# Performance work log

Measured on AMD Instinct MI355X. Metric: run time of the kernel, lower is better.

Reference implementation:

```python
import jax, jax.numpy as jnp
import numpy as np

C = 192
NUM_HEADS = 4
K = 3
KV_STRIDE = 2
EPS = 1e-5


def _conv(x, w, stride, groups):
    # x: [B,C,H,W], w: [O, I//groups, kh, kw]
    return jax.lax.conv_general_dilated(
        x, w, window_strides=(stride, stride),
        padding=[(K // 2, K // 2), (K // 2, K // 2)] if w.shape[-1] > 1 else [(0, 0), (0, 0)],
        dimension_numbers=("NCHW", "OIHW", "NCHW"),
        feature_group_count=groups)


def _bn(x, gamma, beta, mean, var):
    # eval-mode batchnorm over channel dim of NCHW
    inv = gamma / jnp.sqrt(var + EPS)
    return x * inv[None, :, None, None] + (beta - mean * inv)[None, :, None, None]


def _dwconv_flatten(x, dw, g, b, m, v, pw, stride):
    y = _conv(x, dw, stride, groups=C)          # depthwise
    y = _bn(y, g, b, m, v)
    y = _conv(y, pw, 1, groups=1)               # 1x1 pointwise
    B, O, h, w = y.shape
    return y.reshape(B, O, h * w).transpose(0, 2, 1)  # b (h w) c


def setup_inputs() -> dict:
    key = jax.random.key(0)
    ks = jax.random.split(key, 16)
    B, H, W = 8, 56, 56
    d = {
        "x": jax.random.normal(ks[0], (B, H * W, C), jnp.float32),
        "H": H,
        "W": W,
        "dw_q": jax.random.normal(ks[1], (C, 1, K, K), jnp.float32) * 0.1,
        "bn_q_gamma": jax.random.uniform(ks[2], (C,), jnp.float32, 0.5, 1.5),
        "bn_q_beta": jax.random.normal(ks[3], (C,), jnp.float32) * 0.1,
        "bn_q_mean": jax.random.normal(ks[4], (C,), jnp.float32) * 0.1,
        "bn_q_var": jax.random.uniform(ks[5], (C,), jnp.float32, 0.5, 1.5),
        "pw_q": jax.random.normal(ks[6], (C, C, 1, 1), jnp.float32) * (1.0 / np.sqrt(C)),
        "dw_kv": jax.random.normal(ks[7], (C, 1, K, K), jnp.float32) * 0.1,
        "bn_kv_gamma": jax.random.uniform(ks[8], (C,), jnp.float32, 0.5, 1.5),
        "bn_kv_beta": jax.random.normal(ks[9], (C,), jnp.float32) * 0.1,
        "bn_kv_mean": jax.random.normal(ks[10], (C,), jnp.float32) * 0.1,
        "bn_kv_var": jax.random.uniform(ks[11], (C,), jnp.float32, 0.5, 1.5),
        "pw_kv": jax.random.normal(ks[12], (2 * C, C, 1, 1), jnp.float32) * (1.0 / np.sqrt(C)),
        "Wq": jax.random.normal(ks[13], (C, C), jnp.float32) * (1.0 / np.sqrt(C)),
        "bq": jnp.zeros((C,), jnp.float32),
        "Wk": jax.random.normal(ks[14], (C, C), jnp.float32) * (1.0 / np.sqrt(C)),
        "bk": jnp.zeros((C,), jnp.float32),
        "Wv": jax.random.normal(ks[15], (C, C), jnp.float32) * (1.0 / np.sqrt(C)),
        "bv": jnp.zeros((C,), jnp.float32),
    }
    return d


def reference(x, H, W, dw_q, bn_q_gamma, bn_q_beta, bn_q_mean, bn_q_var, pw_q,
              dw_kv, bn_kv_gamma, bn_kv_beta, bn_kv_mean, bn_kv_var, pw_kv,
              Wq, bq, Wk, bk, Wv, bv):
    B, N, _ = x.shape
    h = NUM_HEADS
    hd = C // h
    scale = hd ** -0.5
    # Token2Patch: b (H W) c -> b c H W
    xp = x.transpose(0, 2, 1).reshape(B, C, H, W)
    conv_q = _dwconv_flatten(xp, dw_q, bn_q_gamma, bn_q_beta, bn_q_mean, bn_q_var, pw_q, 1)  # [B,N,C]
    kv = _dwconv_flatten(xp, dw_kv, bn_kv_gamma, bn_kv_beta, bn_kv_mean, bn_kv_var, pw_kv, KV_STRIDE)  # [B,M,2C]
    conv_k, conv_v = kv[..., :C], kv[..., C:]
    q = (conv_q @ Wq.T + bq).reshape(B, N, h, hd).transpose(0, 2, 1, 3)      # [B,h,N,hd]
    M = conv_k.shape[1]
    k = (conv_k @ Wk.T + bk).reshape(B, M, h, hd).transpose(0, 2, 1, 3)      # [B,h,M,hd]
    v = (conv_v @ Wv.T + bv).reshape(B, M, h, hd).transpose(0, 2, 1, 3)      # [B,h,M,hd]
    attn = jnp.einsum("bhnd,bhmd->bhnm", q, k) * scale
    attn = jax.nn.softmax(attn, axis=-1)
    out = jnp.einsum("bhnm,bhmd->bhnd", attn, v)
    # MergeHeads: b h n d -> b n (h d)
    return out.transpose(0, 2, 1, 3).reshape(B, N, C)
```

## Files before the change

### kernel.cpp

```cpp
#include <hip/hip_runtime.h>
#include <cmath>

typedef _Float16 f16;
typedef _Float16 f16x8 __attribute__((ext_vector_type(8)));
typedef _Float16 f16x4 __attribute__((ext_vector_type(4)));
typedef float    f32x4 __attribute__((ext_vector_type(4)));
typedef unsigned int u32;
typedef u32 u32x2 __attribute__((ext_vector_type(2)));

#define C_   192
#define HH   56
#define WW   56
#define NN   3136
#define BB   8
#define MM   784
#define NHEAD 4
#define HD   48
#define VT_LD 832
#define KVPB (BB*MM/32)

#define MFMA16(a,b,c)  __builtin_amdgcn_mfma_f32_16x16x32_f16(a,b,c,0,0,0)
#define MFMAK16(a,b,c) __builtin_amdgcn_mfma_f32_16x16x16f16(a,b,c,0,0,0)

static __device__ __forceinline__ u32 pkrtz(float a, float b) {
    typedef __fp16 fp16x2 __attribute__((ext_vector_type(2)));
    fp16x2 h = __builtin_amdgcn_cvt_pkrtz(a, b);
    return __builtin_bit_cast(u32, h);
}

static __device__ __forceinline__ void gload16(const void* g, void* l) {
    __builtin_amdgcn_global_load_lds(
        (const __attribute__((address_space(1))) unsigned int*)g,
        (__attribute__((address_space(3))) unsigned int*)l, 16, 0, 0);
}

__device__ __forceinline__ void dwbn_oct(
    const float* __restrict__ x, const float* __restrict__ dwL,
    const float* __restrict__ gamma, const float* __restrict__ beta,
    const float* __restrict__ mean,  const float* __restrict__ var,
    f16* __restrict__ out, int idx)
{
    int c4 = idx % 48;
    int r1 = idx / 48;
    int qx = r1 % (WW/4);
    int r2 = r1 / (WW/4);
    int qp = r2 % (HH/2);
    int b  = r2 / (HH/2);
    int c0 = c4*4;

    float4 w4[9];
    #pragma unroll
    for (int j = 0; j < 9; ++j)
        w4[j] = *(const float4*)&dwL[c4*40 + j*4];
    const float* wf = (const float*)w4;

    float4 g4  = *(const float4*)(gamma + c0);
    float4 be4 = *(const float4*)(beta + c0);
    float4 m4  = *(const float4*)(mean + c0);
    float4 v4  = *(const float4*)(var  + c0);

    float4 acc[2][4];
    #pragma unroll
    for (int jj = 0; jj < 2; ++jj)
        #pragma unroll
        for (int ii = 0; ii < 4; ++ii)
            acc[jj][ii] = make_float4(0.f,0.f,0.f,0.f);

    int iyTop = 2*qp - 1;
    int ix0   = 4*qx - 1;
    #pragma unroll
    for (int j = 0; j < 4; ++j) {
        int iy = iyTop + j;
        if (iy < 0 || iy >= HH) continue;
        #pragma unroll
        for (int i = 0; i < 6; ++i) {
            int ix = ix0 + i;
            if (ix < 0 || ix >= WW) continue;
            float4 xv = *reinterpret_cast<const float4*>(
                x + ((size_t)b*NN + iy*WW + ix)*C_ + c0);
            #pragma unroll
            for (int jj = 0; jj < 2; ++jj) {
                if (j < jj || j > jj+2) continue;
                #pragma unroll
                for (int ii = 0; ii < 4; ++ii) {
                    if (i < ii || i > ii+2) continue;
                    const int wi = (j-jj)*3 + (i-ii);
                    acc[jj][ii].x = fmaf(wf[ 0+wi], xv.x, acc[jj][ii].x);
                    acc[jj][ii].y = fmaf(wf[ 9+wi], xv.y, acc[jj][ii].y);
                    acc[jj][ii].z = fmaf(wf[18+wi], xv.z, acc[jj][ii].z);
                    acc[jj][ii].w = fmaf(wf[27+wi], xv.w, acc[jj][ii].w);
                }
            }
        }
    }
    float i0 = g4.x*__frsqrt_rn(v4.x + 1e-5f);
    float i1 = g4.y*__frsqrt_rn(v4.y + 1e-5f);
    float i2 = g4.z*__frsqrt_rn(v4.z + 1e-5f);
    float i3 = g4.w*__frsqrt_rn(v4.w + 1e-5f);
    float b0 = be4.x - m4.x*i0, b1 = be4.y - m4.y*i1;
    float b2 = be4.z - m4.z*i2, b3 = be4.w - m4.w*i3;
    #pragma unroll
    for (int jj = 0; jj < 2; ++jj) {
        #pragma unroll
        for (int ii = 0; ii < 4; ++ii) {
            f16x4 r;
            r[0] = (f16)(acc[jj][ii].x*i0 + b0);
            r[1] = (f16)(acc[jj][ii].y*i1 + b1);
            r[2] = (f16)(acc[jj][ii].z*i2 + b2);
            r[3] = (f16)(acc[jj][ii].w*i3 + b3);
            size_t o = (((size_t)b*HH + 2*qp + jj)*WW + 4*qx + ii)*48 + c4;
            *reinterpret_cast<f16x4*>(out + o*4) = r;
        }
    }
}

__device__ __forceinline__ void dwbn_quad2(
    const float* __restrict__ x, const float* __restrict__ dwL,
    const float* __restrict__ gamma, const float* __restrict__ beta,
    const float* __restrict__ mean,  const float* __restrict__ var,
    f16* __restrict__ out, int idx)
{
    const int OH = 28, OW = 28, STRIDE = 2;
    int c4 = idx % 48;
    int r1 = idx / 48;
    int qx = r1 % (OW/2);
    int r2 = r1 / (OW/2);
    int qp = r2 % (OH/2);
    int b  = r2 / (OH/2);
    int c0 = c4*4;

    float4 w4[9];
    #pragma unroll
    for (int j = 0; j < 9; ++j)
        w4[j] = *(const float4*)&dwL[c4*40 + j*4];
    const float* wf = (const float*)w4;

    float4 g4  = *(const float4*)(gamma + c0);
    float4 be4 = *(const float4*)(beta + c0);
    float4 m4  = *(const float4*)(mean + c0);
    float4 v4  = *(const float4*)(var  + c0);

    float4 a00 = make_float4(0.f,0.f,0.f,0.f);
    float4 a01 = a00, a10 = a00, a11 = a00;
    int iyTop = (2*qp)*STRIDE - 1;
    int ix0   = (2*qx)*STRIDE - 1;
    #pragma unroll
    for (int j = 0; j < STRIDE+3; ++j) {
        int iy = iyTop + j;
        if (iy < 0 || iy >= HH) continue;
        #pragma unroll
        for (int i = 0; i < STRIDE+3; ++i) {
            int ix = ix0 + i;
            if (ix < 0 || ix >= WW) continue;
            float4 xv = *reinterpret_cast<const float4*>(
                x + ((size_t)b*NN + iy*WW + ix)*C_ + c0);
            const bool r0ok = (j <= 2), r1ok = (j >= STRIDE);
            const bool c0ok = (i <= 2), c1ok = (i >= STRIDE);
            if (r0ok && c0ok) { const int wi = j*3 + i;
                a00.x = fmaf(wf[ 0+wi], xv.x, a00.x);
                a00.y = fmaf(wf[ 9+wi], xv.y, a00.y);
                a00.z = fmaf(wf[18+wi], xv.z, a00.z);
                a00.w = fmaf(wf[27+wi], xv.w, a00.w); }
            if (r0ok && c1ok) { const int wi = j*3 + (i-STRIDE);
                a01.x = fmaf(wf[ 0+wi], xv.x, a01.x);
                a01.y = fmaf(wf[ 9+wi], xv.y, a01.y);
                a01.z = fmaf(wf[18+wi], xv.z, a01.z);
                a01.w = fmaf(wf[27+wi], xv.w, a01.w); }
            if (r1ok && c0ok) { const int wi = (j-STRIDE)*3 + i;
                a10.x = fmaf(wf[ 0+wi], xv.x, a10.x);
                a10.y = fmaf(wf[ 9+wi], xv.y, a10.y);
                a10.z = fmaf(wf[18+wi], xv.z, a10.z);
                a10.w = fmaf(wf[27+wi], xv.w, a10.w); }
            if (r1ok && c1ok) { const int wi = (j-STRIDE)*3 + (i-STRIDE);
                a11.x = fmaf(wf[ 0+wi], xv.x, a11.x);
                a11.y = fmaf(wf[ 9+wi], xv.y, a11.y);
                a11.z = fmaf(wf[18+wi], xv.z, a11.z);
                a11.w = fmaf(wf[27+wi], xv.w, a11.w); }
        }
    }
    float i0 = g4.x*__frsqrt_rn(v4.x + 1e-5f);
    float i1 = g4.y*__frsqrt_rn(v4.y + 1e-5f);
    float i2 = g4.z*__frsqrt_rn(v4.z + 1e-5f);
    float i3 = g4.w*__frsqrt_rn(v4.w + 1e-5f);
    float b0 = be4.x - m4.x*i0, b1 = be4.y - m4.y*i1;
    float b2 = be4.z - m4.z*i2, b3 = be4.w - m4.w*i3;
    size_t base = (((size_t)b*OH + 2*qp)*OW + 2*qx)*48 + c4;
    f16x4 r;
    r[0]=(f16)(a00.x*i0+b0); r[1]=(f16)(a00.y*i1+b1);
    r[2]=(f16)(a00.z*i2+b2); r[3]=(f16)(a00.w*i3+b3);
    *reinterpret_cast<f16x4*>(out + base*4) = r;
    r[0]=(f16)(a01.x*i0+b0); r[1]=(f16)(a01.y*i1+b1);
    r[2]=(f16)(a01.z*i2+b2); r[3]=(f16)(a01.w*i3+b3);
    *reinterpret_cast<f16x4*>(out + (base + 48)*4) = r;
    r[0]=(f16)(a10.x*i0+b0); r[1]=(f16)(a10.y*i1+b1);
    r[2]=(f16)(a10.z*i2+b2); r[3]=(f16)(a10.w*i3+b3);
    *reinterpret_cast<f16x4*>(out + (base + (size_t)OW*48)*4) = r;
    r[0]=(f16)(a11.x*i0+b0); r[1]=(f16)(a11.y*i1+b1);
    r[2]=(f16)(a11.z*i2+b2); r[3]=(f16)(a11.w*i3+b3);
    *reinterpret_cast<f16x4*>(out + (base + (size_t)OW*48 + 48)*4) = r;
}

__global__ __launch_bounds__(256) void prep_all(
    const float* __restrict__ x,
    const float* __restrict__ dwq,  const float* __restrict__ gq,
    const float* __restrict__ bq_,  const float* __restrict__ mq,
    const float* __restrict__ vq,
    const float* __restrict__ dwkv, const float* __restrict__ gkv,
    const float* __restrict__ bkv,  const float* __restrict__ mkv,
    const float* __restrict__ vkv,
    const float* __restrict__ Wq, const float* __restrict__ Wk,
    const float* __restrict__ Wv, const float* __restrict__ pw_q,
    const float* __restrict__ pw_kv,
    f16* __restrict__ uq, f16* __restrict__ ukv,
    f16* __restrict__ Mq, f16* __restrict__ Mk, f16* __restrict__ Mv,
    f16* __restrict__ vt)
{
    int blk = blockIdx.x, tid = threadIdx.x;
    const int QB = 588, KB = 294;
    if (blk < QB + KB) {
        bool qp = blk < QB;
        __shared__ __align__(16) float dwL[48*40];
        const float* dwg = qp ? dwq : dwkv;
        for (int i = tid; i < 432; i += 256) {
            int f  = i*4;
            int c4 = f/36, r = f%36;
            *(float4*)&dwL[c4*40 + r] = *(const float4*)(dwg + f);
        }
        __syncthreads();
        if (qp)
            dwbn_oct(x, dwL, gq, bq_, mq, vq, uq, blk*256 + tid);
        else
            dwbn_quad2(x, dwL, gkv, bkv, mkv, vkv, ukv, (blk - QB)*256 + tid);
    } else if (blk < QB + KB + 576) {
        int fb = blk - QB - KB;
        int which = fb / 192, o = fb % 192;
        const float* Wm = which == 0 ? Wq : (which == 1 ? Wk : Wv);
        const float* P  = which == 0 ? pw_q : (which == 1 ? pw_kv : pw_kv + C_*C_);
        f16* Mo         = which == 0 ? Mq : (which == 1 ? Mk : Mv);
        __shared__ float wrow[C_];
        if (tid < C_) wrow[tid] = Wm[o*C_ + tid];
        __syncthreads();
        if (tid < C_) {
            float acc = 0.f;
            #pragma unroll 8
            for (int j = 0; j < C_; ++j)
                acc = fmaf(wrow[j], P[j*C_ + tid], acc);
            Mo[o*C_ + tid] = (f16)acc;
        }
    } else {
        int i = (blk - QB - KB - 576)*256 + tid;
        int b = i / (C_*48);
        int rem = i % (C_*48);
        int c = rem / 48;
        int m = MM + (rem % 48);
        vt[((size_t)b*C_ + c)*VT_LD + m] = (f16)0.f;
    }
}

__global__ __launch_bounds__(128, 1) void proj_kv(
    const f16* __restrict__ ukv,
    const f16* __restrict__ Mk, const f16* __restrict__ Mv,
    const float* __restrict__ bk, const float* __restrict__ bv,
    f16* __restrict__ kb, f16* __restrict__ vt)
{
    int tid  = threadIdx.x;
    int w    = tid >> 6, l = tid & 63;
    int lrow = l & 15,  lgrp = l >> 4;
    int blk  = blockIdx.x;
    int path = blk < KVPB ? 1 : 2;
    int rblk = path == 1 ? blk : blk - KVPB;
    int r0 = rblk*32 + w*16;

    const f16* urow = ukv + (size_t)(r0 + lrow)*C_;
    f16x8 a[6];
    #pragma unroll
    for (int ch = 0; ch < 6; ++ch)
        a[ch] = *(const f16x8*)(urow + ch*32 + lgrp*8);

    f16x8 bfA[6], bfB[6];
    const f16* Mm = path == 1 ? Mk : Mv;

    #pragma unroll
    for (int ch = 0; ch < 6; ++ch)
        bfA[ch] = *(const f16x8*)(Mm + (size_t)lrow*C_ + ch*32 + lgrp*8);

    if (path == 1) {
        #pragma unroll
        for (int ct = 0; ct < 12; ++ct) {
            f16x8* cur = (ct & 1) ? bfB : bfA;
            f16x8* nxt = (ct & 1) ? bfA : bfB;
            if (ct < 11) {
                const f16* mrow = Mm + (size_t)((ct+1)*16 + lrow)*C_;
                #pragma unroll
                for (int ch = 0; ch < 6; ++ch)
                    nxt[ch] = *(const f16x8*)(mrow + ch*32 + lgrp*8);
            }
            f32x4 acc = {0.f,0.f,0.f,0.f};
            #pragma unroll
            for (int ch = 0; ch < 6; ++ch)
                acc = MFMA16(cur[ch], a[ch], acc);
            float4 bo = *(const float4*)(bk + ct*16 + lgrp*4);
            f16x4 st;
            st[0] = (f16)(acc[0] + bo.x);
            st[1] = (f16)(acc[1] + bo.y);
            st[2] = (f16)(acc[2] + bo.z);
            st[3] = (f16)(acc[3] + bo.w);
            *(f16x4*)(kb + (size_t)(r0 + lrow)*C_ + ct*16 + lgrp*4) = st;
        }
    } else {
        #pragma unroll
        for (int ct = 0; ct < 12; ++ct) {
            f16x8* cur = (ct & 1) ? bfB : bfA;
            f16x8* nxt = (ct & 1) ? bfA : bfB;
            if (ct < 11) {
                const f16* mrow = Mv + (size_t)((ct+1)*16 + lrow)*C_;
                #pragma unroll
                for (int ch = 0; ch < 6; ++ch)
                    nxt[ch] = *(const f16x8*)(mrow + ch*32 + lgrp*8);
            }
            int o = ct*16 + lrow;
            f32x4 acc = {0.f,0.f,0.f,0.f};
            #pragma unroll
            for (int ch = 0; ch < 6; ++ch)
                acc = MFMA16(a[ch], cur[ch], acc);
            float bo = bv[o];
            int rg = r0 + lgrp*4;
            int b  = rg / MM, m = rg % MM;
            f16x4 st;
            st[0] = (f16)(acc[0] + bo);
            st[1] = (f16)(acc[1] + bo);
            st[2] = (f16)(acc[2] + bo);
            st[3] = (f16)(acc[3] + bo);
            *(f16x4*)(vt + ((size_t)b*C_ + o)*VT_LD + m) = st;
        }
    }
}

__device__ __forceinline__ void stage_tile(
    int w, int l, f16* ldsKb, f16* ldsVb,
    const f16* __restrict__ kbb, const f16* __restrict__ vbb, int m0)
{
    int rr = l >> 3, p = l & 7;
    #pragma unroll
    for (int j = 0; j < 4; ++j) {
        int u = w + j*4;
        if (u < 8) {
            int r = u*8 + rr;
            int c = p ^ (r & 7);
            gload16(kbb + (size_t)(m0 + r)*C_ + c*8, ldsKb + u*512);
        } else if (u < 14) {
            int d = (u-8)*8 + rr;
            int c = p ^ (d & 7);
            gload16(vbb + (size_t)d*VT_LD + m0 + c*8, ldsVb + (u-8)*512);
        }
    }
}

__device__ __forceinline__ float softmax_upd(
    f32x4* s, float& mrun, float& lrun, u32* pk)
{
    float t0 = fmaxf(fmaxf(s[0][0], s[0][1]), fmaxf(s[0][2], s[0][3]));
    float t1 = fmaxf(fmaxf(s[1][0], s[1][1]), fmaxf(s[1][2], s[1][3]));
    float t2 = fmaxf(fmaxf(s[2][0], s[2][1]), fmaxf(s[2][2], s[2][3]));
    float t3 = fmaxf(fmaxf(s[3][0], s[3][1]), fmaxf(s[3][2], s[3][3]));
    float tmax = fmaxf(fmaxf(t0, t1), fmaxf(t2, t3));
    tmax = fmaxf(tmax, __shfl_xor(tmax, 16));
    tmax = fmaxf(tmax, __shfl_xor(tmax, 32));
    float mnew = fmaxf(mrun, tmax);
    float corr = exp2f(mrun - mnew);
    mrun = mnew;
    float psum = 0.f;
    #pragma unroll
    for (int j = 0; j < 4; ++j) {
        #pragma unroll
        for (int r = 0; r < 4; ++r) {
            s[j][r] = exp2f(s[j][r] - mnew);
            psum += s[j][r];
        }
    }
    lrun = lrun*corr + psum;
    #pragma unroll
    for (int j = 0; j < 4; ++j) {
        pk[j*2]   = pkrtz(s[j][0], s[j][1]);
        pk[j*2+1] = pkrtz(s[j][2], s[j][3]);
    }
    return corr;
}

__device__ __forceinline__ void compute_tile64(
    const f16* ldsKb, const f16* ldsVb,
    const f16x8& qf0, const f16x4& qfh,
    float& mrun, float& lrun, f32x4& o0, f32x4& o1, f32x4& o2,
    int lrow, int g, bool tail)
{
    const char* kP = (const char*)ldsKb;
    const char* vP = (const char*)ldsVb;
    f32x4 z = {0.f,0.f,0.f,0.f};
    int sw = lrow & 7;
    int cA = (g ^ sw) << 4;
    int cH = (((4 + (g >> 1)) ^ sw) << 4) + ((g & 1) << 3);

    f32x4 s[4];
    __builtin_amdgcn_s_setprio(1);
    #pragma unroll
    for (int j = 0; j < 4; ++j) {
        const char* rb = kP + (16*j + lrow)*128;
        f32x4 t = MFMA16(*(const f16x8*)(rb + cA), qf0, z);
        s[j] = MFMAK16(*(const f16x4*)(rb + cH), qfh, t);
    }
    __builtin_amdgcn_s_setprio(0);

    if (tail) {
        f32x4 neg = {-1e30f,-1e30f,-1e30f,-1e30f};
        s[1] = neg; s[2] = neg; s[3] = neg;
    }

    u32 pk[8];
    float corr = softmax_upd(s, mrun, lrun, pk);

    #pragma unroll
    for (int r = 0; r < 4; ++r) { o0[r] *= corr; o1[r] *= corr; o2[r] *= corr; }

    #pragma unroll
    for (int ch = 0; ch < 4; ++ch) {
        u32x2 pw = { pk[2*ch], pk[2*ch+1] };
        f16x4 pb = __builtin_bit_cast(f16x4, pw);
        int off = (((2*ch + (g >> 1)) ^ sw) << 4) + ((g & 1) << 3);
        f16x4 v0 = *(const f16x4*)(vP + lrow*128      + off);
        f16x4 v1 = *(const f16x4*)(vP + (16+lrow)*128 + off);
        f16x4 v2 = *(const f16x4*)(vP + (32+lrow)*128 + off);
        __builtin_amdgcn_s_setprio(1);
        o0 = MFMAK16(v0, pb, o0);
        o1 = MFMAK16(v1, pb, o1);
        o2 = MFMAK16(v2, pb, o2);
        __builtin_amdgcn_s_setprio(0);
    }
}

__global__ __launch_bounds__(256, 2) void attn_mfma(
    const f16* __restrict__ uq, const f16* __restrict__ Mq,
    const float* __restrict__ bq,
    const f16* __restrict__ kb, const f16* __restrict__ vt,
    float* __restrict__ out)
{
    __shared__ __align__(16) f16 ldsK[2][64*64];
    __shared__ __align__(16) f16 ldsV[2][48*64];
    __shared__ __align__(16) f16 qL[4][16*56];

    int tid  = threadIdx.x;
    int w    = tid >> 6, l = tid & 63;
    int lrow = l & 15,  g = l >> 4;
    int swz  = (blockIdx.x & 7)*196 + (blockIdx.x >> 3);
    int bh   = swz / 49, qblk = swz % 49;
    int h    = bh & 3, b = bh >> 2;
    int n0   = qblk*64 + w*16;

    const f16* kbb = kb + (size_t)b*MM*C_ + h*HD;
    const f16* vbb = vt + ((size_t)b*C_ + h*HD)*VT_LD;

    const f16* urow = uq + ((size_t)b*NN + n0 + lrow)*C_;
    f16x8 ufr[6];
    #pragma unroll
    for (int ch = 0; ch < 6; ++ch)
        ufr[ch] = *(const f16x8*)(urow + ch*32 + g*8);

    stage_tile(w, l, &ldsK[0][0], &ldsV[0][0], kbb, vbb, 0);

    {
        const float qsc = 0.14433756729740643f * 1.4426950408889634f;
        f16* qw = &qL[w][0];
        #pragma unroll
        for (int dt = 0; dt < 3; ++dt) {
            const f16* mrow = Mq + (size_t)(h*HD + dt*16 + lrow)*C_;
            f32x4 acc = {0.f,0.f,0.f,0.f};
            #pragma unroll
            for (int ch = 0; ch < 6; ++ch)
                acc = MFMA16(*(const f16x8*)(mrow + ch*32 + g*8), ufr[ch], acc);
            float4 bo = *(const float4*)(bq + h*HD + dt*16 + g*4);
            f16x4 st;
            st[0] = (f16)((acc[0] + bo.x)*qsc);
            st[1] = (f16)((acc[1] + bo.y)*qsc);
            st[2] = (f16)((acc[2] + bo.z)*qsc);
            st[3] = (f16)((acc[3] + bo.w)*qsc);
            *(f16x4*)(qw + lrow*56 + dt*16 + g*4) = st;
        }
    }
    f16x8 qf0 = *(const f16x8*)(&qL[w][0] + lrow*56 + g*8);
    f16x4 qfh = *(const f16x4*)(&qL[w][0] + lrow*56 + 32 + g*4);
    asm volatile("" :: "v"(qf0), "v"(qfh));

    float mrun = -1e30f, lrun = 0.f;
    f32x4 o0 = {0.f,0.f,0.f,0.f}, o1 = o0, o2 = o0;

    for (int t = 0; t < 13; ++t) {
        int nb = t & 1;
        if (t < 12)
            stage_tile(w, l, &ldsK[nb^1][0], &ldsV[nb^1][0], kbb, vbb, (t+1)*64);
        __builtin_amdgcn_sched_barrier(0);
        if (t < 12) {
            if (w < 2) asm volatile("s_waitcnt vmcnt(4)" ::: "memory");
            else       asm volatile("s_waitcnt vmcnt(3)" ::: "memory");
        } else {
            asm volatile("s_waitcnt vmcnt(0)" ::: "memory");
        }
        __builtin_amdgcn_s_barrier();
        __builtin_amdgcn_sched_barrier(0);
        compute_tile64(&ldsK[nb][0], &ldsV[nb][0], qf0, qfh,
                       mrun, lrun, o0, o1, o2, lrow, g, t == 12);
        __builtin_amdgcn_sched_barrier(0);
        __builtin_amdgcn_s_barrier();
    }

    lrun += __shfl_xor(lrun, 16);
    lrun += __shfl_xor(lrun, 32);
    float inv = 1.f / lrun;
    f32x4 r0, r1, r2;
    #pragma unroll
    for (int r = 0; r < 4; ++r) {
        r0[r] = o0[r]*inv; r1[r] = o1[r]*inv; r2[r] = o2[r]*inv;
    }
    float* obase = out + ((size_t)b*NN + n0 + lrow)*C_ + h*HD + g*4;
    *(f32x4*)(obase)      = r0;
    *(f32x4*)(obase + 16) = r1;
    *(f32x4*)(obase + 32) = r2;
}

extern "C" void kernel_launch(void* const* d_in, const int* in_sizes, int n_in,
                              void* d_out, int out_size, void* d_ws, size_t ws_size,
                              hipStream_t stream)
{
    const float* x     = (const float*)d_in[0];
    const float* dw_q  = (const float*)d_in[3];
    const float* bnqg  = (const float*)d_in[4];
    const float* bnqb  = (const float*)d_in[5];
    const float* bnqm  = (const float*)d_in[6];
    const float* bnqv  = (const float*)d_in[7];
    const float* pw_q  = (const float*)d_in[8];
    const float* dw_kv = (const float*)d_in[9];
    const float* bnkg  = (const float*)d_in[10];
    const float* bnkb  = (const float*)d_in[11];
    const float* bnkm  = (const float*)d_in[12];
    const float* bnkvv = (const float*)d_in[13];
    const float* pw_kv = (const float*)d_in[14];
    const float* Wq    = (const float*)d_in[15];
    const float* bq    = (const float*)d_in[16];
    const float* Wk    = (const float*)d_in[17];
    const float* bk    = (const float*)d_in[18];
    const float* Wv    = (const float*)d_in[19];
    const float* bv    = (const float*)d_in[20];
    float* out = (float*)d_out;

    f16* p   = (f16*)d_ws;
    f16* Mq16  = p;  p += C_*C_;
    f16* Mk16  = p;  p += C_*C_;
    f16* Mv16  = p;  p += C_*C_;
    f16* uq16  = p;  p += (size_t)BB*NN*C_ + 256;
    f16* ukv16 = p;  p += (size_t)BB*MM*C_;
    f16* kb16  = p;  p += (size_t)BB*MM*C_ + 16384;
    f16* vt16  = p;  p += (size_t)BB*C_*VT_LD;

    prep_all<<<1746, 256, 0, stream>>>(
        x, dw_q, bnqg, bnqb, bnqm, bnqv,
        dw_kv, bnkg, bnkb, bnkm, bnkvv,
        Wq, Wk, Wv, pw_q, pw_kv,
        uq16, ukv16, Mq16, Mk16, Mv16, vt16);

    proj_kv<<<2*KVPB, 128, 0, stream>>>(
        ukv16, Mk16, Mv16, bk, bv, kb16, vt16);

    attn_mfma<<<1568, 256, 0, stream>>>(uq16, Mq16, bq, kb16, vt16, out);
}
```

Measured before the change: 97.80 us.

## Add lazy softmax rescaling and alias Q staging buffer into K LDS

Adds a wave-uniform fast path that skips the running-max shuffle reduction and the output rescale when every lane's tile max stays within a threshold of the stored max. Exponentials are then taken against the stale max. Separately, the Q scratch buffer now overlays the second K buffer to cut LDS footprint, with a barrier before the first tile is staged. This lowers per-tile softmax ALU and cross-lane work and may raise occupancy, but it adds a divergent branch, removes the overlap of the first tile load with the Q projection, and relies on exponent headroom for fp16 probabilities.

```diff
diff --git a/kernel.cpp b/kernel.cpp
--- a/kernel.cpp
+++ b/kernel.cpp
@@ -356,42 +356,20 @@
     }
 }
 
-__device__ __forceinline__ float softmax_upd(
-    f32x4* s, float& mrun, float& lrun, u32* pk)
+__device__ __forceinline__ float max16(const f32x4* s)
 {
     float t0 = fmaxf(fmaxf(s[0][0], s[0][1]), fmaxf(s[0][2], s[0][3]));
     float t1 = fmaxf(fmaxf(s[1][0], s[1][1]), fmaxf(s[1][2], s[1][3]));
     float t2 = fmaxf(fmaxf(s[2][0], s[2][1]), fmaxf(s[2][2], s[2][3]));
     float t3 = fmaxf(fmaxf(s[3][0], s[3][1]), fmaxf(s[3][2], s[3][3]));
-    float tmax = fmaxf(fmaxf(t0, t1), fmaxf(t2, t3));
-    tmax = fmaxf(tmax, __shfl_xor(tmax, 16));
-    tmax = fmaxf(tmax, __shfl_xor(tmax, 32));
-    float mnew = fmaxf(mrun, tmax);
-    float corr = exp2f(mrun - mnew);
-    mrun = mnew;
-    float psum = 0.f;
-    #pragma unroll
-    for (int j = 0; j < 4; ++j) {
-        #pragma unroll
-        for (int r = 0; r < 4; ++r) {
-            s[j][r] = exp2f(s[j][r] - mnew);
-            psum += s[j][r];
-        }
-    }
-    lrun = lrun*corr + psum;
-    #pragma unroll
-    for (int j = 0; j < 4; ++j) {
-        pk[j*2]   = pkrtz(s[j][0], s[j][1]);
-        pk[j*2+1] = pkrtz(s[j][2], s[j][3]);
-    }
-    return corr;
+    return fmaxf(fmaxf(t0, t1), fmaxf(t2, t3));
 }
 
 __device__ __forceinline__ void compute_tile64(
     const f16* ldsKb, const f16* ldsVb,
     const f16x8& qf0, const f16x4& qfh,
     float& mrun, float& lrun, f32x4& o0, f32x4& o1, f32x4& o2,
-    int lrow, int g, bool tail)
+    int lrow, int g, bool first, bool tail)
 {
     const char* kP = (const char*)ldsKb;
     const char* vP = (const char*)ldsVb;
@@ -416,10 +394,53 @@
     }
 
     u32 pk[8];
-    float corr = softmax_upd(s, mrun, lrun, pk);
-
-    #pragma unroll
-    for (int r = 0; r < 4; ++r) { o0[r] *= corr; o1[r] *= corr; o2[r] *= corr; }
+    float tl = max16(s);
+    bool fast = false;
+    if (!first) fast = (__all(tl <= mrun + 8.0f) != 0);
+
+    if (fast) {
+        float psum = 0.f;
+        #pragma unroll
+        for (int j = 0; j < 4; ++j) {
+            #pragma unroll
+            for (int r = 0; r < 4; ++r) {
+                s[j][r] = exp2f(s[j][r] - mrun);
+                psum += s[j][r];
+            }
+        }
+        lrun += psum;
+        #pragma unroll
+        for (int j = 0; j < 4; ++j) {
+            pk[j*2]   = pkrtz(s[j][0], s[j][1]);
+            pk[j*2+1] = pkrtz(s[j][2], s[j][3]);
+        }
+    } else {
+        float tmax = tl;
+        tmax = fmaxf(tmax, __shfl_xor(tmax, 16));
+        tmax = fmaxf(tmax, __shfl_xor(tmax, 32));
+        float mnew = fmaxf(mrun, tmax);
+        float corr = exp2f(mrun - mnew);
+        mrun = mnew;
+        float psum = 0.f;
+        #pragma unroll
+        for (int j = 0; j < 4; ++j) {
+            #pragma unroll
+            for (int r = 0; r < 4; ++r) {
+                s[j][r] = exp2f(s[j][r] - mnew);
+                psum += s[j][r];
+            }
+        }
+        lrun = lrun*corr + psum;
+        #pragma unroll
+        for (int j = 0; j < 4; ++j) {
+            pk[j*2]   = pkrtz(s[j][0], s[j][1]);
+            pk[j*2+1] = pkrtz(s[j][2], s[j][3]);
+        }
+        #pragma unroll
+        for (int r = 0; r < 4; ++r) {
+            o0[r] *= corr; o1[r] *= corr; o2[r] *= corr;
+        }
+    }
 
     #pragma unroll
     for (int ch = 0; ch < 4; ++ch) {
@@ -443,9 +464,12 @@
     const f16* __restrict__ kb, const f16* __restrict__ vt,
     float* __restrict__ out)
 {
-    __shared__ __align__(16) f16 ldsK[2][64*64];
-    __shared__ __align__(16) f16 ldsV[2][48*64];
-    __shared__ __align__(16) f16 qL[4][16*56];
+    __shared__ __align__(16) f16 lds[2*4096 + 2*3072];
+    f16* ldsK0 = lds;
+    f16* ldsK1 = lds + 4096;
+    f16* ldsV0 = lds + 8192;
+    f16* ldsV1 = lds + 8192 + 3072;
+    f16* qL    = ldsK1;
 
     int tid  = threadIdx.x;
     int w    = tid >> 6, l = tid & 63;
@@ -463,12 +487,9 @@
     #pragma unroll
     for (int ch = 0; ch < 6; ++ch)
         ufr[ch] = *(const f16x8*)(urow + ch*32 + g*8);
-
-    stage_tile(w, l, &ldsK[0][0], &ldsV[0][0], kbb, vbb, 0);
-
     {
         const float qsc = 0.14433756729740643f * 1.4426950408889634f;
-        f16* qw = &qL[w][0];
+        f16* qw = qL + w*896;
         #pragma unroll
         for (int dt = 0; dt < 3; ++dt) {
             const f16* mrow = Mq + (size_t)(h*HD + dt*16 + lrow)*C_;
@@ -485,9 +506,12 @@
             *(f16x4*)(qw + lrow*56 + dt*16 + g*4) = st;
         }
     }
-    f16x8 qf0 = *(const f16x8*)(&qL[w][0] + lrow*56 + g*8);
-    f16x4 qfh = *(const f16x4*)(&qL[w][0] + lrow*56 + 32 + g*4);
+    f16x8 qf0 = *(const f16x8*)(qL + w*896 + lrow*56 + g*8);
+    f16x4 qfh = *(const f16x4*)(qL + w*896 + lrow*56 + 32 + g*4);
     asm volatile("" :: "v"(qf0), "v"(qfh));
+    __builtin_amdgcn_s_barrier();
+
+    stage_tile(w, l, ldsK0, ldsV0, kbb, vbb, 0);
 
     float mrun = -1e30f, lrun = 0.f;
     f32x4 o0 = {0.f,0.f,0.f,0.f}, o1 = o0, o2 = o0;
@@ -495,7 +519,8 @@
     for (int t = 0; t < 13; ++t) {
         int nb = t & 1;
         if (t < 12)
-            stage_tile(w, l, &ldsK[nb^1][0], &ldsV[nb^1][0], kbb, vbb, (t+1)*64);
+            stage_tile(w, l, nb ? ldsK0 : ldsK1, nb ? ldsV0 : ldsV1,
+                       kbb, vbb, (t+1)*64);
         __builtin_amdgcn_sched_barrier(0);
         if (t < 12) {
             if (w < 2) asm volatile("s_waitcnt vmcnt(4)" ::: "memory");
@@ -505,8 +530,8 @@
         }
         __builtin_amdgcn_s_barrier();
         __builtin_amdgcn_sched_barrier(0);
-        compute_tile64(&ldsK[nb][0], &ldsV[nb][0], qf0, qfh,
-                       mrun, lrun, o0, o1, o2, lrow, g, t == 12);
+        compute_tile64(nb ? ldsK1 : ldsK0, nb ? ldsV1 : ldsV0, qf0, qfh,
+                       mrun, lrun, o0, o1, o2, lrow, g, t == 0, t == 12);
         __builtin_amdgcn_sched_barrier(0);
         __builtin_amdgcn_s_barrier();
     }
```

Result: faster. 95.04 us, median of 2 (-2.8%).
